# Optimization experiments

Hardware: AMD Instinct MI355X
Metric: run time of the kernel (lower is better)

Reference implementation:

```python
import jax, jax.numpy as jnp
import numpy as np

EPS = 1e-6        # eigenvalue clamp for numerical safety (matrices are well-conditioned by construction)
MOMENTUM = 0.1    # init kwarg


def _sym_apply(X, fn):
    """Apply a spectral function to a batch of symmetric matrices via eigh."""
    w, V = jnp.linalg.eigh(X)
    w = jnp.maximum(w, EPS)
    return jnp.einsum('...ij,...j,...kj->...ik', V, fn(w), V)


def sqrtm(X):
    return _sym_apply(X, jnp.sqrt)


def invsqrtm(X):
    return _sym_apply(X, lambda w: 1.0 / jnp.sqrt(w))


def logm(X):
    return _sym_apply(X, jnp.log)


def expm_sym(X):
    w, V = jnp.linalg.eigh(X)
    return jnp.einsum('...ij,...j,...kj->...ik', V, jnp.exp(w), V)


def powm(X, t):
    return _sym_apply(X, lambda w: w ** t)


def congr_neg(X, G):
    """CongrG(X, G, 'neg') = G^{-1/2} X G^{-1/2}, broadcast over batch dims of X."""
    Gi = invsqrtm(G)
    return jnp.einsum('ij,...jk,kl->...il', Gi, X, Gi)


def bary_geom(Xm):
    """Karcher (Frechet) mean of SPD matrices Xm: (N, n, n).
    One Karcher-flow step initialized at the arithmetic mean (SPDNet-BN convention)."""
    G = jnp.mean(Xm, axis=0)
    Gs, Gi = sqrtm(G), invsqrtm(G)
    L = logm(jnp.einsum('ij,bjk,kl->bil', Gi, Xm, Gi))   # log-maps at G
    return Gs @ expm_sym(jnp.mean(L, axis=0)) @ Gs


def geodesic(A, B, t):
    """SPD geodesic from A toward B at time t: A^{1/2} (A^{-1/2} B A^{-1/2})^t A^{1/2}."""
    As, Ai = sqrtm(A), invsqrtm(A)
    return As @ powm(Ai @ B @ Ai, t) @ As


def setup_inputs() -> dict:
    key = jax.random.key(0)
    N, T, V, M, n = 32, 64, 25, 2, 16
    A = jax.random.normal(key, (N, T, V, M, n, n), dtype=jnp.float32)
    # SPD construction: A A^T / n + 0.5 I  (min eigenvalue >= 0.5)
    X = jnp.einsum('...ij,...kj->...ik', A, A) / n + 0.5 * jnp.eye(n, dtype=jnp.float32)
    running_mean = jnp.eye(n, dtype=jnp.float32)  # torch.eye(n) in __init__
    return {"X": X, "running_mean": running_mean}


def reference(X, running_mean):
    N, T, V, M, n, _ = X.shape
    Xf = X.reshape(N, T * V * M, n, n)
    X_mean = jnp.mean(Xf, axis=1)                      # (N, n, n) per-sample arithmetic mean
    mean = bary_geom(X_mean)                           # (n, n) Karcher mean over batch
    new_running_mean = geodesic(running_mean, mean, MOMENTUM)  # no_grad EMA in torch
    X_centered = congr_neg(Xf, mean)                   # mean^{-1/2} X mean^{-1/2}
    return X_centered.reshape(N, T, V, M, n, n), new_running_mean
```

## Files before the change

kernel.cpp:

```cpp
#include <hip/hip_runtime.h>
#include <math.h>

#define NS     32
#define BBATCH 3200
#define NMAT   102400
#define EPSC   1e-6f
#define ST     20
#define IX(i,j) ((i)*ST+(j))
#define MSZ    (16*ST)

#define PART_O 0
#define XM_O   131072
#define GS_O   139264
#define GI_O   139520
#define L_O    139776
#define MEAN_O 147968
#define WI_O   148224
#define RS_O   148480
#define RI_O   148736


__device__ __forceinline__ void g2l(const float* __restrict__ g, float* l, int t) {
  if (t < 64) {
    int i = t >> 2, j0 = (t & 3) << 2;
    *(float4*)&l[IX(i, j0)] = *(const float4*)&g[i * 16 + j0];
  }
  __syncthreads();
}

__device__ __forceinline__ void l2g(const float* l, float* __restrict__ g, int t) {
  if (t < 64) {
    int i = t >> 2, j0 = (t & 3) << 2;
    *(float4*)&g[i * 16 + j0] = *(const float4*)&l[IX(i, j0)];
  }
  __syncthreads();
}

__device__ __forceinline__ void mm(const float* A, const float* B, float* C, int t) {
  if (t < 64) {
    int i = t >> 2, j0 = (t & 3) << 2;
    float4 acc = make_float4(0.f, 0.f, 0.f, 0.f);
    #pragma unroll
    for (int k = 0; k < 16; ++k) {
      float a = A[IX(i, k)];
      const float4 b = *(const float4*)&B[IX(k, j0)];
      acc.x += a * b.x; acc.y += a * b.y; acc.z += a * b.z; acc.w += a * b.w;
    }
    *(float4*)&C[IX(i, j0)] = acc;
  }
  __syncthreads();
}

__device__ __forceinline__ void mad_diag(float* C, float s, float d, int t) {
  if (t < 64) {
    int i = t >> 2, j0 = (t & 3) << 2;
    float4 p = *(float4*)&C[IX(i, j0)];
    p.x *= s; p.y *= s; p.z *= s; p.w *= s;
    if (i == j0) p.x += d; else if (i == j0 + 1) p.y += d;
    else if (i == j0 + 2) p.z += d; else if (i == j0 + 3) p.w += d;
    *(float4*)&C[IX(i, j0)] = p;
  }
  __syncthreads();
}

__device__ __forceinline__ void set_scaled_I(float* C, float d, int t) {
  if (t < 64) {
    int i = t >> 2, j0 = (t & 3) << 2;
    float4 p = make_float4(0.f, 0.f, 0.f, 0.f);
    if (i == j0) p.x = d; else if (i == j0 + 1) p.y = d;
    else if (i == j0 + 2) p.z = d; else if (i == j0 + 3) p.w = d;
    *(float4*)&C[IX(i, j0)] = p;
  }
  __syncthreads();
}

__device__ __forceinline__ void symmetrize(float* A, int t) {
  float4 v = make_float4(0.f, 0.f, 0.f, 0.f);
  if (t < 64) {
    int i = t >> 2, j0 = (t & 3) << 2;
    float4 a = *(float4*)&A[IX(i, j0)];
    v.x = 0.5f * (a.x + A[IX(j0,     i)]);
    v.y = 0.5f * (a.y + A[IX(j0 + 1, i)]);
    v.z = 0.5f * (a.z + A[IX(j0 + 2, i)]);
    v.w = 0.5f * (a.w + A[IX(j0 + 3, i)]);
  }
  __syncthreads();
  if (t < 64) {
    int i = t >> 2, j0 = (t & 3) << 2;
    *(float4*)&A[IX(i, j0)] = v;
  }
  __syncthreads();
}

__device__ __forceinline__ float trace16(const float* A) {
  float tr = 0.f;
  #pragma unroll
  for (int k = 0; k < 16; ++k) tr += A[IX(k, k)];
  return tr;
}

#define NS_IT 8
__device__ void ns_sqrtm(const float* A, float* Y0, float* Y1, float* Z0, float* Z1,
                         float* P, int t, float** pS, float** pZ) {
  float c = trace16(A) * (1.f / 16.f);
  float ic = 1.f / c;
  if (t < 64) {
    int i = t >> 2, j0 = (t & 3) << 2;
    float4 a = *(const float4*)&A[IX(i, j0)];
    a.x *= ic; a.y *= ic; a.z *= ic; a.w *= ic;
    *(float4*)&Y0[IX(i, j0)] = a;
    float4 z = make_float4(0.f, 0.f, 0.f, 0.f);
    if (i == j0) z.x = 1.f; else if (i == j0 + 1) z.y = 1.f;
    else if (i == j0 + 2) z.z = 1.f; else if (i == j0 + 3) z.w = 1.f;
    *(float4*)&Z0[IX(i, j0)] = z;
  }
  __syncthreads();
  float *Y = Y0, *Yn = Y1, *Z = Z0, *Zn = Z1;
  for (int it = 0; it < NS_IT; ++it) {
    mm(Z, Y, P, t);
    mad_diag(P, -0.5f, 1.5f, t);
    mm(Y, P, Yn, t);
    mm(P, Z, Zn, t);
    float* tp = Y; Y = Yn; Yn = tp;
    tp = Z; Z = Zn; Zn = tp;
  }
  float sc = sqrtf(c), isc = 1.f / sc;
  if (t < 64) {
    int i = t >> 2, j0 = (t & 3) << 2;
    float4 y = *(float4*)&Y[IX(i, j0)];
    y.x *= sc; y.y *= sc; y.z *= sc; y.w *= sc;
    *(float4*)&Y[IX(i, j0)] = y;
    float4 z = *(float4*)&Z[IX(i, j0)];
    z.x *= isc; z.y *= isc; z.z *= isc; z.w *= isc;
    *(float4*)&Z[IX(i, j0)] = z;
  }
  __syncthreads();
  *pS = Y; *pZ = Z;
}

#define LOG_M 12
__device__ void logm_taylor(float* S, float* L, float* R0, float* R1, int t) {
  mad_diag(S, 1.f, -1.f, t);
  float am = ((LOG_M & 1) ? 1.f : -1.f) / (float)LOG_M;
  set_scaled_I(R0, am, t);
  float *R = R0, *Rn = R1;
  for (int j = LOG_M - 1; j >= 1; --j) {
    mm(S, R, Rn, t);
    float aj = ((j & 1) ? 1.f : -1.f) / (float)j;
    mad_diag(Rn, 1.f, aj, t);
    float* tp = R; R = Rn; Rn = tp;
  }
  mm(S, R, L, t);
}

#define EXP_M 10
__device__ float* expm_taylor(const float* K, float* R0, float* R1, int t) {
  set_scaled_I(R0, 1.f, t);
  float *R = R0, *Rn = R1;
  for (int j = EXP_M; j >= 1; --j) {
    mm(K, R, Rn, t);
    mad_diag(Rn, 1.f / (float)j, 1.f, t);
    float* tp = R; R = Rn; Rn = tp;
  }
  return R;
}


__global__ __launch_bounds__(256) void k_part(const float* __restrict__ X, float* __restrict__ ws) {
  int b = blockIdx.x >> 4;
  int c = blockIdx.x & 15;
  int t = threadIdx.x;
  int e4 = t & 63;
  int r  = t >> 6;
  const float4* X4 = (const float4*)X;
  float4 s = make_float4(0.f, 0.f, 0.f, 0.f);
  long mbase = (long)b * BBATCH + c * 200;
  for (int i = r; i < 200; i += 4) {
    float4 v = X4[(mbase + i) * 64 + e4];
    s.x += v.x; s.y += v.y; s.z += v.z; s.w += v.w;
  }
  __shared__ float4 red[256];
  red[t] = s;
  __syncthreads();
  if (t < 64) {
    float4 a = red[t], b1 = red[t + 64], c1 = red[t + 128], d = red[t + 192];
    float4 o;
    o.x = a.x + b1.x + c1.x + d.x;
    o.y = a.y + b1.y + c1.y + d.y;
    o.z = a.z + b1.z + c1.z + d.z;
    o.w = a.w + b1.w + c1.w + d.w;
    ((float4*)(ws + PART_O))[(long)blockIdx.x * 64 + t] = o;
  }
}

__global__ __launch_bounds__(256) void k_xm(float* __restrict__ ws) {
  int b = blockIdx.x, t = threadIdx.x;
  float a = 0.f;
  for (int c = 0; c < 16; ++c) a += ws[PART_O + (b * 16 + c) * 256 + t];
  ws[XM_O + b * 256 + t] = a * (1.f / BBATCH);
}

__global__ __launch_bounds__(64) void k_prep(const float* __restrict__ rm, float* __restrict__ ws) {
  __shared__ __align__(16) float A[MSZ], Y0[MSZ], Y1[MSZ], Z0[MSZ], Z1[MSZ], P[MSZ];
  int t = threadIdx.x;
  if (blockIdx.x == 0) {
    if (t < 64) {
      int i = t >> 2, j0 = (t & 3) << 2;
      float4 a = make_float4(0.f, 0.f, 0.f, 0.f);
      for (int b = 0; b < NS; ++b) {
        float4 v = *(const float4*)&ws[XM_O + b * 256 + i * 16 + j0];
        a.x += v.x; a.y += v.y; a.z += v.z; a.w += v.w;
      }
      float s = 1.f / NS;
      a.x *= s; a.y *= s; a.z *= s; a.w *= s;
      *(float4*)&A[IX(i, j0)] = a;
    }
    __syncthreads();
  } else {
    g2l(rm, A, t);
  }
  float *S, *Z;
  ns_sqrtm(A, Y0, Y1, Z0, Z1, P, t, &S, &Z);
  l2g(S, ws + (blockIdx.x == 0 ? GS_O : RS_O), t);
  l2g(Z, ws + (blockIdx.x == 0 ? GI_O : RI_O), t);
}

__global__ __launch_bounds__(64) void k_logmap(float* __restrict__ ws) {
  __shared__ __align__(16) float Gi[MSZ], Xb[MSZ], S[MSZ], T[MSZ], R0[MSZ], R1[MSZ];
  int b = blockIdx.x, t = threadIdx.x;
  g2l(ws + GI_O, Gi, t);
  g2l(ws + XM_O + b * 256, Xb, t);
  mm(Gi, Xb, T, t);
  mm(T, Gi, S, t);
  symmetrize(S, t);
  logm_taylor(S, T, R0, R1, t);
  l2g(T, ws + L_O + b * 256, t);
}

__global__ __launch_bounds__(64) void k_mean2(float* __restrict__ ws) {
  __shared__ __align__(16) float K[MSZ], Gs[MSZ], T1[MSZ], T2[MSZ], R0[MSZ], R1[MSZ], P[MSZ];
  int t = threadIdx.x;
  if (t < 64) {
    int i = t >> 2, j0 = (t & 3) << 2;
    float4 a = make_float4(0.f, 0.f, 0.f, 0.f);
    for (int b = 0; b < NS; ++b) {
      float4 v = *(const float4*)&ws[L_O + b * 256 + i * 16 + j0];
      a.x += v.x; a.y += v.y; a.z += v.z; a.w += v.w;
    }
    float s = 1.f / NS;
    a.x *= s; a.y *= s; a.z *= s; a.w *= s;
    *(float4*)&K[IX(i, j0)] = a;
  }
  __syncthreads();
  float* E = expm_taylor(K, R0, R1, t);
  g2l(ws + GS_O, Gs, t);
  mm(Gs, E, T1, t);
  mm(T1, Gs, T2, t);
  symmetrize(T2, t);
  l2g(T2, ws + MEAN_O, t);
  float *S, *Z;
  ns_sqrtm(T2, R0, R1, T1, K, P, t, &S, &Z);
  l2g(Z, ws + WI_O, t);
}

__global__ __launch_bounds__(256) void k_center(const float* __restrict__ X,
                                                const float* __restrict__ ws,
                                                float* __restrict__ out) {
  __shared__ __align__(16) float B0[MSZ], B1[MSZ], B2[MSZ], B3[MSZ], B4[MSZ];
  __shared__ __align__(16) float Xs[4 * MSZ];
  __shared__ __align__(16) float Ts[4 * MSZ];
  __shared__ __align__(16) float Wsm[MSZ];
  int t = threadIdx.x;

  if (blockIdx.x == 0) {
    g2l(ws + RI_O, B0, t);
    g2l(ws + MEAN_O, B1, t);
    mm(B0, B1, B2, t);
    mm(B2, B0, B1, t);
    symmetrize(B1, t);
    float c = trace16(B1) * (1.f / 16.f);
    mad_diag(B1, 1.f / c, 0.f, t);
    logm_taylor(B1, B2, B3, B4, t);
    mad_diag(B2, 0.1f, 0.f, t);
    float* Ep = expm_taylor(B2, B3, B4, t);
    float s = expf(0.1f * logf(c));
    mad_diag(Ep, s, 0.f, t);
    g2l(ws + RS_O, B1, t);
    mm(B1, Ep, B2, t);
    mm(B2, B1, B4, t);
    l2g(B4, out + (size_t)NMAT * 256, t);
  } else {
    long m0 = (long)(blockIdx.x - 1) * 4;
    Wsm[(t >> 4) * ST + (t & 15)] = ws[WI_O + t];
    const float4* X4 = (const float4*)X;
    float4 xv = X4[m0 * 64 + t];
    int mm_ = t >> 6;
    int l  = t & 63;
    int i  = l >> 2;
    int j0 = (l & 3) << 2;
    *(float4*)&Xs[mm_ * MSZ + i * ST + j0] = xv;
    __syncthreads();
    float4 a = make_float4(0.f, 0.f, 0.f, 0.f);
    #pragma unroll
    for (int k = 0; k < 16; ++k) {
      float x = Xs[mm_ * MSZ + i * ST + k];
      const float4 wv = *(const float4*)&Wsm[k * ST + j0];
      a.x += x * wv.x; a.y += x * wv.y; a.z += x * wv.z; a.w += x * wv.w;
    }
    *(float4*)&Ts[mm_ * MSZ + i * ST + j0] = a;
    __syncthreads();
    float4 y = make_float4(0.f, 0.f, 0.f, 0.f);
    #pragma unroll
    for (int k = 0; k < 16; ++k) {
      float w = Wsm[i * ST + k];
      const float4 tv = *(const float4*)&Ts[mm_ * MSZ + k * ST + j0];
      y.x += w * tv.x; y.y += w * tv.y; y.z += w * tv.z; y.w += w * tv.w;
    }
    ((float4*)out)[m0 * 64 + t] = y;
  }
}

extern "C" void kernel_launch(void* const* d_in, const int* in_sizes, int n_in,
                              void* d_out, int out_size, void* d_ws, size_t ws_size,
                              hipStream_t stream) {
  (void)in_sizes; (void)n_in; (void)out_size; (void)ws_size;
  const float* X  = (const float*)d_in[0];
  const float* rm = (const float*)d_in[1];
  float* out = (float*)d_out;
  float* ws  = (float*)d_ws;

  k_part   <<<dim3(512),   dim3(256), 0, stream>>>(X, ws);
  k_xm     <<<dim3(32),    dim3(256), 0, stream>>>(ws);
  k_prep   <<<dim3(2),     dim3(64),  0, stream>>>(rm, ws);
  k_logmap <<<dim3(32),    dim3(64),  0, stream>>>(ws);
  k_mean2  <<<dim3(1),     dim3(64),  0, stream>>>(ws);
  k_center <<<dim3(25601), dim3(256), 0, stream>>>(X, ws, out);
}
```

Before: 246.4 us.

## Register-tile center kernel, fold k_xm into k_prep, cut series iterations

Rewrites the congruence kernel so each 8-thread group handles one matrix with two rows per thread, holding W^{-1/2} rows and intermediate products in registers. Each block now covers 32 matrices, giving far fewer blocks and fewer syncs. The k_xm reduction is merged into k_prep, removing one launch. Newton-Schulz, log-Taylor and exp-Taylor iteration counts are lowered, which trades accuracy in the small serial kernels for less latency.

Result: slower. 260.5 us (+5.8%).

```diff
diff --git a/kernel.cpp b/kernel.cpp
--- a/kernel.cpp
+++ b/kernel.cpp
@@ -19,6 +19,10 @@
 #define RS_O   148480
 #define RI_O   148736
 
+#define NS_IT  5
+#define LOG_M  8
+#define EXP_M  8
+
 
 __device__ __forceinline__ void g2l(const float* __restrict__ g, float* l, int t) {
   if (t < 64) {
@@ -99,7 +103,6 @@
   return tr;
 }
 
-#define NS_IT 8
 __device__ void ns_sqrtm(const float* A, float* Y0, float* Y1, float* Z0, float* Z1,
                          float* P, int t, float** pS, float** pZ) {
   float c = trace16(A) * (1.f / 16.f);
@@ -138,7 +141,6 @@
   *pS = Y; *pZ = Z;
 }
 
-#define LOG_M 12
 __device__ void logm_taylor(float* S, float* L, float* R0, float* R1, int t) {
   mad_diag(S, 1.f, -1.f, t);
   float am = ((LOG_M & 1) ? 1.f : -1.f) / (float)LOG_M;
@@ -153,7 +155,6 @@
   mm(S, R, L, t);
 }
 
-#define EXP_M 10
 __device__ float* expm_taylor(const float* K, float* R0, float* R1, int t) {
   set_scaled_I(R0, 1.f, t);
   float *R = R0, *Rn = R1;
@@ -193,17 +194,18 @@
   }
 }
 
-__global__ __launch_bounds__(256) void k_xm(float* __restrict__ ws) {
-  int b = blockIdx.x, t = threadIdx.x;
-  float a = 0.f;
-  for (int c = 0; c < 16; ++c) a += ws[PART_O + (b * 16 + c) * 256 + t];
-  ws[XM_O + b * 256 + t] = a * (1.f / BBATCH);
-}
-
-__global__ __launch_bounds__(64) void k_prep(const float* __restrict__ rm, float* __restrict__ ws) {
+__global__ __launch_bounds__(256) void k_prep(const float* __restrict__ rm, float* __restrict__ ws) {
   __shared__ __align__(16) float A[MSZ], Y0[MSZ], Y1[MSZ], Z0[MSZ], Z1[MSZ], P[MSZ];
   int t = threadIdx.x;
   if (blockIdx.x == 0) {
+    for (int o = t; o < NS * 256; o += 256) {
+      int b = o >> 8, e = o & 255;
+      float a = 0.f;
+      for (int c = 0; c < 16; ++c) a += ws[PART_O + (b * 16 + c) * 256 + e];
+      ws[XM_O + o] = a * (1.f / BBATCH);
+    }
+    __threadfence_block();
+    __syncthreads();
     if (t < 64) {
       int i = t >> 2, j0 = (t & 3) << 2;
       float4 a = make_float4(0.f, 0.f, 0.f, 0.f);
@@ -263,16 +265,19 @@
   l2g(Z, ws + WI_O, t);
 }
 
+#define SLAB 324
 __global__ __launch_bounds__(256) void k_center(const float* __restrict__ X,
                                                 const float* __restrict__ ws,
                                                 float* __restrict__ out) {
-  __shared__ __align__(16) float B0[MSZ], B1[MSZ], B2[MSZ], B3[MSZ], B4[MSZ];
-  __shared__ __align__(16) float Xs[4 * MSZ];
-  __shared__ __align__(16) float Ts[4 * MSZ];
-  __shared__ __align__(16) float Wsm[MSZ];
+  __shared__ __align__(16) float lds[32 * SLAB];
   int t = threadIdx.x;
 
   if (blockIdx.x == 0) {
+    float* B0 = &lds[0];
+    float* B1 = &lds[MSZ];
+    float* B2 = &lds[2 * MSZ];
+    float* B3 = &lds[3 * MSZ];
+    float* B4 = &lds[4 * MSZ];
     g2l(ws + RI_O, B0, t);
     g2l(ws + MEAN_O, B1, t);
     mm(B0, B1, B2, t);
@@ -289,34 +294,81 @@
     mm(B1, Ep, B2, t);
     mm(B2, B1, B4, t);
     l2g(B4, out + (size_t)NMAT * 256, t);
-  } else {
-    long m0 = (long)(blockIdx.x - 1) * 4;
-    Wsm[(t >> 4) * ST + (t & 15)] = ws[WI_O + t];
-    const float4* X4 = (const float4*)X;
-    float4 xv = X4[m0 * 64 + t];
-    int mm_ = t >> 6;
-    int l  = t & 63;
-    int i  = l >> 2;
-    int j0 = (l & 3) << 2;
-    *(float4*)&Xs[mm_ * MSZ + i * ST + j0] = xv;
-    __syncthreads();
-    float4 a = make_float4(0.f, 0.f, 0.f, 0.f);
-    #pragma unroll
-    for (int k = 0; k < 16; ++k) {
-      float x = Xs[mm_ * MSZ + i * ST + k];
-      const float4 wv = *(const float4*)&Wsm[k * ST + j0];
-      a.x += x * wv.x; a.y += x * wv.y; a.z += x * wv.z; a.w += x * wv.w;
-    }
-    *(float4*)&Ts[mm_ * MSZ + i * ST + j0] = a;
-    __syncthreads();
-    float4 y = make_float4(0.f, 0.f, 0.f, 0.f);
-    #pragma unroll
-    for (int k = 0; k < 16; ++k) {
-      float w = Wsm[i * ST + k];
-      const float4 tv = *(const float4*)&Ts[mm_ * MSZ + k * ST + j0];
-      y.x += w * tv.x; y.y += w * tv.y; y.z += w * tv.z; y.w += w * tv.w;
-    }
-    ((float4*)out)[m0 * 64 + t] = y;
+    return;
+  }
+
+  int w  = t >> 6;
+  int l  = t & 63;
+  int mw = l >> 3;
+  int r  = l & 7;
+  long m = (long)(blockIdx.x - 1) * 32 + w * 8 + mw;
+  const float* __restrict__ Wg = ws + WI_O;
+
+  float wr[2][16];
+  #pragma unroll
+  for (int h = 0; h < 2; ++h) {
+    #pragma unroll
+    for (int c = 0; c < 4; ++c) {
+      float4 v = ((const float4*)Wg)[(r + 8 * h) * 4 + c];
+      wr[h][4 * c] = v.x; wr[h][4 * c + 1] = v.y; wr[h][4 * c + 2] = v.z; wr[h][4 * c + 3] = v.w;
+    }
+  }
+
+  float* slab = &lds[(w * 8 + mw) * SLAB];
+  const float4* X4 = (const float4*)X;
+  #pragma unroll
+  for (int h = 0; h < 2; ++h) {
+    #pragma unroll
+    for (int c = 0; c < 4; ++c) {
+      float4 v = X4[m * 64 + (r + 8 * h) * 4 + c];
+      *(float4*)&slab[(r + 8 * h) * ST + 4 * c] = v;
+    }
+  }
+  asm volatile("s_waitcnt lgkmcnt(0)" ::: "memory");
+
+  float u[2][16];
+  #pragma unroll
+  for (int h = 0; h < 2; ++h)
+    #pragma unroll
+    for (int j = 0; j < 16; ++j) u[h][j] = 0.f;
+  #pragma unroll
+  for (int k = 0; k < 16; ++k) {
+    float4 b0 = *(const float4*)&slab[k * ST + 0];
+    float4 b1 = *(const float4*)&slab[k * ST + 4];
+    float4 b2 = *(const float4*)&slab[k * ST + 8];
+    float4 b3 = *(const float4*)&slab[k * ST + 12];
+    #pragma unroll
+    for (int h = 0; h < 2; ++h) {
+      float a = wr[h][k];
+      u[h][0]  += a * b0.x; u[h][1]  += a * b0.y; u[h][2]  += a * b0.z; u[h][3]  += a * b0.w;
+      u[h][4]  += a * b1.x; u[h][5]  += a * b1.y; u[h][6]  += a * b1.z; u[h][7]  += a * b1.w;
+      u[h][8]  += a * b2.x; u[h][9]  += a * b2.y; u[h][10] += a * b2.z; u[h][11] += a * b2.w;
+      u[h][12] += a * b3.x; u[h][13] += a * b3.y; u[h][14] += a * b3.z; u[h][15] += a * b3.w;
+    }
+  }
+
+  float y[2][16];
+  #pragma unroll
+  for (int h = 0; h < 2; ++h)
+    #pragma unroll
+    for (int j = 0; j < 16; ++j) y[h][j] = 0.f;
+  #pragma unroll
+  for (int k = 0; k < 16; ++k) {
+    #pragma unroll
+    for (int j = 0; j < 16; ++j) {
+      float wkj = Wg[k * 16 + j];
+      y[0][j] += u[0][k] * wkj;
+      y[1][j] += u[1][k] * wkj;
+    }
+  }
+
+  #pragma unroll
+  for (int h = 0; h < 2; ++h) {
+    #pragma unroll
+    for (int c = 0; c < 4; ++c) {
+      float4 v = make_float4(y[h][4 * c], y[h][4 * c + 1], y[h][4 * c + 2], y[h][4 * c + 3]);
+      *(float4*)&out[m * 256 + (r + 8 * h) * 16 + 4 * c] = v;
+    }
   }
 }
 
@@ -329,10 +381,9 @@
   float* out = (float*)d_out;
   float* ws  = (float*)d_ws;
 
-  k_part   <<<dim3(512),   dim3(256), 0, stream>>>(X, ws);
-  k_xm     <<<dim3(32),    dim3(256), 0, stream>>>(ws);
-  k_prep   <<<dim3(2),     dim3(64),  0, stream>>>(rm, ws);
-  k_logmap <<<dim3(32),    dim3(64),  0, stream>>>(ws);
-  k_mean2  <<<dim3(1),     dim3(64),  0, stream>>>(ws);
-  k_center <<<dim3(25601), dim3(256), 0, stream>>>(X, ws, out);
-}
+  k_part   <<<dim3(512),  dim3(256), 0, stream>>>(X, ws);
+  k_prep   <<<dim3(2),    dim3(256), 0, stream>>>(rm, ws);
+  k_logmap <<<dim3(32),   dim3(64),  0, stream>>>(ws);
+  k_mean2  <<<dim3(1),    dim3(64),  0, stream>>>(ws);
+  k_center <<<dim3(3201), dim3(256), 0, stream>>>(X, ws, out);
+}
```
